# Performance work log

Hardware: AMD Instinct MI355X
Metric: run time of the kernel (lower is better)

The kernel has to match this reference:

```python
import jax, jax.numpy as jnp
import numpy as np


def _bicubic_warp(img, dx, dy):
    """Faithful JAX port of Warp_Object.forward with flag='bicubic'.
    img: [B,C,H,W] float32; dx, dy: [B,1,H,W] pixel displacements.
    Replicates the original tile-order quirk: X/Y are repeated C times along
    dim0 (order c*B+b) while the image is flattened in b*C+c order.
    """
    B, C, H, W = img.shape
    Wm1 = jnp.float32(max(W - 1, 1))
    Hm1 = jnp.float32(max(H - 1, 1))
    xs = jnp.arange(W, dtype=jnp.float32)
    ys = jnp.arange(H, dtype=jnp.float32)
    Xg, Yg = jnp.meshgrid(xs, ys)          # [H,W]
    # normalized grid in [-1,1] as in forward()
    newX = 2.0 * (Xg[None] + dx[:, 0]) / Wm1 - 1.0   # [B,H,W]
    newY = 2.0 * (Yg[None] + dy[:, 0]) / Hm1 - 1.0
    # repeat over channels exactly like X.repeat([C,1,1,1]) (tile order)
    x_map = (jnp.tile(newX, (C, 1, 1)) + 1.0) * Wm1 / 2.0   # [B*C,H,W]
    y_map = (jnp.tile(newY, (C, 1, 1)) + 1.0) * Hm1 / 2.0

    x0 = jnp.floor(x_map)
    y0 = jnp.floor(y_map)
    tx = x_map - x0
    ty = y_map - y0

    def cubic_coeffs(t):
        cm1 = (-t ** 3 + 2.0 * t ** 2 - t) / 2.0
        c0 = (3.0 * t ** 3 - 5.0 * t ** 2 + 2.0) / 2.0
        c1 = (-3.0 * t ** 3 + 4.0 * t ** 2 + t) / 2.0
        c2 = 1.0 - (cm1 + c0 + c1)
        return (cm1, c0, c1, c2)

    cx = cubic_coeffs(tx)
    cy = cubic_coeffs(ty)

    x0i = x0.astype(jnp.int32)
    y0i = y0.astype(jnp.int32)
    xi = [jnp.clip(x0i + o, 0, W - 1) for o in (-1, 0, 1, 2)]
    yi = [jnp.clip(y0i + o, 0, H - 1) for o in (-1, 0, 1, 2)]

    flat = img.reshape(B * C, H, W)
    row = jnp.arange(B * C)[:, None, None]   # per-image base offset

    out = jnp.zeros_like(x_map)
    for j in range(4):            # 4 rows of the 4x4 bicubic stencil
        row_acc = jnp.zeros_like(x_map)
        for i in range(4):
            row_acc = row_acc + cx[i] * flat[row, yi[j], xi[i]]
        out = out + cy[j] * row_acc
    return out.reshape(B, C, H, W)


def setup_inputs() -> dict:
    key = jax.random.key(0)
    k1, k2, k3 = jax.random.split(key, 3)
    B, C, H, W = 4, 3, 512, 512
    input_image = jax.random.normal(k1, (B, C, H, W), dtype=jnp.float32)
    delta_x = jax.random.normal(k2, (B, 1, H, W), dtype=jnp.float32) * 1.5
    delta_y = jax.random.normal(k3, (B, 1, H, W), dtype=jnp.float32) * 1.5
    return {"input_image": input_image, "delta_x": delta_x, "delta_y": delta_y}


def reference(input_image, delta_x, delta_y):
    return _bicubic_warp(input_image, delta_x, delta_y)
```

## Files before the change

kernel.cpp:

```cpp
#include <hip/hip_runtime.h>


constexpr int B = 4, C = 3, H = 512, W = 512;
constexpr int HW = H * W;
constexpr int TH2 = 32, TW = 32;
constexpr int HALO = 6;
constexpr int RS = TH2 + 2 * HALO;
constexpr int LSTC = 48;
constexpr int CHR = LSTC / 4;
constexpr int NCH = RS * CHR;
constexpr int CPW = NCH / 16;
constexpr int TDW = RS * LSTC;
constexpr int NT = 1024;
constexpr int NB = B * (H / TH2) * (W / TW);

typedef float f4 __attribute__((ext_vector_type(4)));
typedef f4 f4u __attribute__((aligned(4)));

typedef const __attribute__((address_space(1))) void* gas_t;
typedef __attribute__((address_space(3))) void* las_t;

__device__ __forceinline__ void gload_lds16(const float* g, float* l) {
    __builtin_amdgcn_global_load_lds((gas_t)g, (las_t)l, 16, 0, 0);
}

__global__ __launch_bounds__(NT, 8)
void warp_bicubic_gen(const float* __restrict__ img,
                      const float* __restrict__ dxp,
                      const float* __restrict__ dyp,
                      float* __restrict__ out)
{
    __shared__ float tile[C][TDW];

    int b   = blockIdx.x;
    int swz = (b & 7) * (NB / 8) + (b >> 3);
    int bd  = swz >> 8;
    int ty  = (swz >> 4) & 15;
    int tx  = swz & 15;
    int yb  = ty * TH2;
    int xb  = tx * TW;
    int cb  = min(max(xb - HALO, 0), W - LSTC);

    int tid  = threadIdx.x;
    int wv   = tid >> 6;
    int lane = tid & 63;
    int ry   = wv * 2 + (lane >> 5);
    int cidx = lane & 31;
    int y    = yb + ry;
    int x    = xb + cidx;
    int pixoff = y * W + x;

    float dxv = __builtin_nontemporal_load(dxp + bd * HW + pixoff);
    float dyv = __builtin_nontemporal_load(dyp + bd * HW + pixoff);

    if (lane < CPW) {
        int chunk = wv * CPW + lane;
        int r  = chunk / CHR;
        int c4 = (chunk - r * CHR) * 4;
        int sr = min(max(yb - HALO + r, 0), H - 1);
        int soff = sr * W + cb + c4;
        const float* g0 = img + (size_t)bd * HW + soff;
        float* l0 = &tile[0][chunk * 4];
        gload_lds16(g0,           l0);
        gload_lds16(g0 + 4 * HW,  l0 + TDW);
        gload_lds16(g0 + 8 * HW,  l0 + 2 * TDW);
    }

    float xm = (float)x + dxv;
    float ym = (float)y + dyv;
    float x0f = floorf(xm), y0f = floorf(ym);
    float ftx = xm - x0f, fty = ym - y0f;
    int x0 = (int)x0f, y0 = (int)y0f;
    int s  = min(max(x0 - 1, 0), W - 4);

    float tx2 = ftx * ftx, tx3 = tx2 * ftx;
    float cx0 = (-tx3 + 2.0f * tx2 - ftx) * 0.5f;
    float cx1 = (3.0f * tx3 - 5.0f * tx2 + 2.0f) * 0.5f;
    float cx2 = (-3.0f * tx3 + 4.0f * tx2 + ftx) * 0.5f;
    float cx3 = 1.0f - (cx0 + cx1 + cx2);

    float ty2 = fty * fty, ty3 = ty2 * fty;
    float cy0 = (-ty3 + 2.0f * ty2 - fty) * 0.5f;
    float cy1 = (3.0f * ty3 - 5.0f * ty2 + 2.0f) * 0.5f;
    float cy2 = (-3.0f * ty3 + 4.0f * ty2 + fty) * 0.5f;
    float cy3 = 1.0f - (cy0 + cy1 + cy2);

    float w0, w1, w2, w3;
    if (__builtin_expect(x0 >= 1 && x0 <= W - 3, 1)) {
        w0 = cx0; w1 = cx1; w2 = cx2; w3 = cx3;
    } else {
        w0 = w1 = w2 = w3 = 0.f;
        const float cxa[4] = {cx0, cx1, cx2, cx3};
#pragma unroll
        for (int o = 0; o < 4; ++o) {
            int xi = min(max(x0 - 1 + o, 0), W - 1);
            int e  = xi - s;
            float cc = cxa[o];
            w0 += (e == 0) ? cc : 0.f;
            w1 += (e == 1) ? cc : 0.f;
            w2 += (e == 2) ? cc : 0.f;
            w3 += (e == 3) ? cc : 0.f;
        }
    }

    unsigned rel = (unsigned)(y0 - (yb - HALO + 1));
    unsigned lsv = (unsigned)(s - cb);
    bool intile = (rel <= (unsigned)(RS - 4)) & (lsv <= (unsigned)(LSTC - 4));
    int lbase = (int)rel * LSTC + (int)lsv;

    __syncthreads();

#pragma unroll
    for (int c = 0; c < C; ++c) {
        int kp = bd + 4 * c;
        const float* __restrict__ tp = &tile[c][0];
        float acc;
        if (__builtin_expect(intile, 1)) {
            const float* rp = tp + lbase;
            float r0 = cy0 * (w0 * rp[0] + w1 * rp[1] + w2 * rp[2] + w3 * rp[3]);
            rp += LSTC;
            float r1 = cy1 * (w0 * rp[0] + w1 * rp[1] + w2 * rp[2] + w3 * rp[3]);
            rp += LSTC;
            float r2 = cy2 * (w0 * rp[0] + w1 * rp[1] + w2 * rp[2] + w3 * rp[3]);
            rp += LSTC;
            float r3 = cy3 * (w0 * rp[0] + w1 * rp[1] + w2 * rp[2] + w3 * rp[3]);
            acc = (r0 + r1) + (r2 + r3);
        } else {
            const float* __restrict__ plane = img + (size_t)kp * HW;
            const float cya[4] = {cy0, cy1, cy2, cy3};
            acc = 0.f;
#pragma unroll
            for (int j = 0; j < 4; ++j) {
                int yi = min(max(y0 - 1 + j, 0), H - 1);
                f4 v = *(const f4u*)(plane + yi * W + s);
                acc += cya[j] * (w0 * v.x + w1 * v.y + w2 * v.z + w3 * v.w);
            }
        }
        __builtin_nontemporal_store(acc, out + (size_t)kp * HW + pixoff);
    }
}

extern "C" void kernel_launch(void* const* d_in, const int* in_sizes, int n_in,
                              void* d_out, int out_size, void* d_ws, size_t ws_size,
                              hipStream_t stream) {
    const float* img = (const float*)d_in[0];
    const float* dx  = (const float*)d_in[1];
    const float* dy  = (const float*)d_in[2];
    float* out = (float*)d_out;

    dim3 block(NT);
    dim3 grid(NB);
    hipLaunchKernelGGL(warp_bicubic_gen, grid, block, 0, stream,
                       img, dx, dy, out);
}
```

Measured before the change: 16.11 us.

## Process two vertically stacked tiles per block with double-buffered LDS staging

Each workgroup now covers two adjacent 32x32 tiles, halving the grid to 512 blocks. Both tiles' image halos are issued to LDS asynchronously up front, into separate buffers. Partial vmcnt waits let the first tile's stencil run while the second tile's loads are still in flight. This aims to hide global-load latency and amortise per-block setup, at the cost of fewer blocks to spread across CUs, reloading the halo rows the two tiles share, and fragile hand-counted waitcnt logic.

```diff
diff --git a/kernel.cpp b/kernel.cpp
--- a/kernel.cpp
+++ b/kernel.cpp
@@ -3,16 +3,16 @@
 
 constexpr int B = 4, C = 3, H = 512, W = 512;
 constexpr int HW = H * W;
-constexpr int TH2 = 32, TW = 32;
+constexpr int TS = 32;
 constexpr int HALO = 6;
-constexpr int RS = TH2 + 2 * HALO;
+constexpr int RS = TS + 2 * HALO;
 constexpr int LSTC = 48;
 constexpr int CHR = LSTC / 4;
 constexpr int NCH = RS * CHR;
 constexpr int CPW = NCH / 16;
 constexpr int TDW = RS * LSTC;
 constexpr int NT = 1024;
-constexpr int NB = B * (H / TH2) * (W / TW);
+constexpr int NB = 512;
 
 typedef float f4 __attribute__((ext_vector_type(4)));
 typedef f4 f4u __attribute__((aligned(4)));
@@ -24,48 +24,17 @@
     __builtin_amdgcn_global_load_lds((gas_t)g, (las_t)l, 16, 0, 0);
 }
 
-__global__ __launch_bounds__(NT, 8)
-void warp_bicubic_gen(const float* __restrict__ img,
-                      const float* __restrict__ dxp,
-                      const float* __restrict__ dyp,
-                      float* __restrict__ out)
-{
-    __shared__ float tile[C][TDW];
-
-    int b   = blockIdx.x;
-    int swz = (b & 7) * (NB / 8) + (b >> 3);
-    int bd  = swz >> 8;
-    int ty  = (swz >> 4) & 15;
-    int tx  = swz & 15;
-    int yb  = ty * TH2;
-    int xb  = tx * TW;
-    int cb  = min(max(xb - HALO, 0), W - LSTC);
-
-    int tid  = threadIdx.x;
-    int wv   = tid >> 6;
-    int lane = tid & 63;
-    int ry   = wv * 2 + (lane >> 5);
-    int cidx = lane & 31;
-    int y    = yb + ry;
-    int x    = xb + cidx;
-    int pixoff = y * W + x;
-
-    float dxv = __builtin_nontemporal_load(dxp + bd * HW + pixoff);
-    float dyv = __builtin_nontemporal_load(dyp + bd * HW + pixoff);
-
-    if (lane < CPW) {
-        int chunk = wv * CPW + lane;
-        int r  = chunk / CHR;
-        int c4 = (chunk - r * CHR) * 4;
-        int sr = min(max(yb - HALO + r, 0), H - 1);
-        int soff = sr * W + cb + c4;
-        const float* g0 = img + (size_t)bd * HW + soff;
-        float* l0 = &tile[0][chunk * 4];
-        gload_lds16(g0,           l0);
-        gload_lds16(g0 + 4 * HW,  l0 + TDW);
-        gload_lds16(g0 + 8 * HW,  l0 + 2 * TDW);
-    }
-
+struct Coef {
+    float w0, w1, w2, w3;
+    float cy0, cy1, cy2, cy3;
+    int   lbase;
+    bool  intile;
+    int   y0, s;
+};
+
+__device__ __forceinline__ Coef make_coef(int x, int y, float dxv, float dyv,
+                                          int yb, int cb) {
+    Coef cf;
     float xm = (float)x + dxv;
     float ym = (float)y + dyv;
     float x0f = floorf(xm), y0f = floorf(ym);
@@ -76,20 +45,19 @@
     float tx2 = ftx * ftx, tx3 = tx2 * ftx;
     float cx0 = (-tx3 + 2.0f * tx2 - ftx) * 0.5f;
     float cx1 = (3.0f * tx3 - 5.0f * tx2 + 2.0f) * 0.5f;
-    float cx2 = (-3.0f * tx3 + 4.0f * tx2 + ftx) * 0.5f;
+    float cx2 = (-tx3 * 3.0f + 4.0f * tx2 + ftx) * 0.5f;
     float cx3 = 1.0f - (cx0 + cx1 + cx2);
 
     float ty2 = fty * fty, ty3 = ty2 * fty;
-    float cy0 = (-ty3 + 2.0f * ty2 - fty) * 0.5f;
-    float cy1 = (3.0f * ty3 - 5.0f * ty2 + 2.0f) * 0.5f;
-    float cy2 = (-3.0f * ty3 + 4.0f * ty2 + fty) * 0.5f;
-    float cy3 = 1.0f - (cy0 + cy1 + cy2);
-
-    float w0, w1, w2, w3;
+    cf.cy0 = (-ty3 + 2.0f * ty2 - fty) * 0.5f;
+    cf.cy1 = (3.0f * ty3 - 5.0f * ty2 + 2.0f) * 0.5f;
+    cf.cy2 = (-3.0f * ty3 + 4.0f * ty2 + fty) * 0.5f;
+    cf.cy3 = 1.0f - (cf.cy0 + cf.cy1 + cf.cy2);
+
     if (__builtin_expect(x0 >= 1 && x0 <= W - 3, 1)) {
-        w0 = cx0; w1 = cx1; w2 = cx2; w3 = cx3;
+        cf.w0 = cx0; cf.w1 = cx1; cf.w2 = cx2; cf.w3 = cx3;
     } else {
-        w0 = w1 = w2 = w3 = 0.f;
+        float w0 = 0.f, w1 = 0.f, w2 = 0.f, w3 = 0.f;
         const float cxa[4] = {cx0, cx1, cx2, cx3};
 #pragma unroll
         for (int o = 0; o < 4; ++o) {
@@ -101,42 +69,122 @@
             w2 += (e == 2) ? cc : 0.f;
             w3 += (e == 3) ? cc : 0.f;
         }
+        cf.w0 = w0; cf.w1 = w1; cf.w2 = w2; cf.w3 = w3;
     }
 
     unsigned rel = (unsigned)(y0 - (yb - HALO + 1));
     unsigned lsv = (unsigned)(s - cb);
-    bool intile = (rel <= (unsigned)(RS - 4)) & (lsv <= (unsigned)(LSTC - 4));
-    int lbase = (int)rel * LSTC + (int)lsv;
-
-    __syncthreads();
+    cf.intile = (rel <= (unsigned)(RS - 4)) & (lsv <= (unsigned)(LSTC - 4));
+    cf.lbase  = (int)rel * LSTC + (int)lsv;
+    cf.y0 = y0; cf.s = s;
+    return cf;
+}
+
+__device__ __forceinline__ float stencil1(const float* __restrict__ tp,
+                                          const Coef& cf,
+                                          const float* __restrict__ plane) {
+    if (__builtin_expect(cf.intile, 1)) {
+        const float* rp = tp + cf.lbase;
+        float r0 = cf.cy0 * (cf.w0 * rp[0] + cf.w1 * rp[1] + cf.w2 * rp[2] + cf.w3 * rp[3]);
+        rp += LSTC;
+        float r1 = cf.cy1 * (cf.w0 * rp[0] + cf.w1 * rp[1] + cf.w2 * rp[2] + cf.w3 * rp[3]);
+        rp += LSTC;
+        float r2 = cf.cy2 * (cf.w0 * rp[0] + cf.w1 * rp[1] + cf.w2 * rp[2] + cf.w3 * rp[3]);
+        rp += LSTC;
+        float r3 = cf.cy3 * (cf.w0 * rp[0] + cf.w1 * rp[1] + cf.w2 * rp[2] + cf.w3 * rp[3]);
+        return (r0 + r1) + (r2 + r3);
+    } else {
+        const float cya[4] = {cf.cy0, cf.cy1, cf.cy2, cf.cy3};
+        float acc = 0.f;
+#pragma unroll
+        for (int j = 0; j < 4; ++j) {
+            int yi = min(max(cf.y0 - 1 + j, 0), H - 1);
+            f4 v = *(const f4u*)(plane + yi * W + cf.s);
+            acc += cya[j] * (cf.w0 * v.x + cf.w1 * v.y + cf.w2 * v.z + cf.w3 * v.w);
+        }
+        return acc;
+    }
+}
+
+__device__ __forceinline__ void stage_tile(const float* __restrict__ img, int bd,
+                                           int yb, int cb, float* dst,
+                                           int wv, int lane) {
+    if (lane < CPW) {
+        int chunk = wv * CPW + lane;
+        int r  = chunk / CHR;
+        int c4 = (chunk - r * CHR) * 4;
+        int sr = min(max(yb - HALO + r, 0), H - 1);
+        int soff = sr * W + cb + c4;
+        const float* g0 = img + (size_t)bd * HW + soff;
+        float* l0 = dst + chunk * 4;
+        gload_lds16(g0,          l0);
+        gload_lds16(g0 + 4 * HW, l0 + TDW);
+        gload_lds16(g0 + 8 * HW, l0 + 2 * TDW);
+    }
+}
+
+__global__ __launch_bounds__(NT, 8)
+void warp_bicubic_2t(const float* __restrict__ img,
+                     const float* __restrict__ dxp,
+                     const float* __restrict__ dyp,
+                     float* __restrict__ out)
+{
+    __shared__ float tile[2][C * TDW];
+
+    int b   = blockIdx.x;
+    int swz = (b & 7) * (NB / 8) + (b >> 3);
+    int bd  = swz >> 7;
+    int rem = swz & 127;
+    int typ = rem >> 4;
+    int txx = rem & 15;
+    int xb  = txx * TS;
+    int cb  = min(max(xb - HALO, 0), W - LSTC);
+    int yb0 = typ * 2 * TS;
+    int yb1 = yb0 + TS;
+
+    int tid  = threadIdx.x;
+    int wv   = tid >> 6;
+    int lane = tid & 63;
+    int ry   = wv * 2 + (lane >> 5);
+    int cidx = lane & 31;
+    int x    = xb + cidx;
+    int po0  = (yb0 + ry) * W + x;
+    int po1  = (yb1 + ry) * W + x;
+
+    float dx0 = __builtin_nontemporal_load(dxp + bd * HW + po0);
+    float dy0 = __builtin_nontemporal_load(dyp + bd * HW + po0);
+    float dx1 = __builtin_nontemporal_load(dxp + bd * HW + po1);
+    float dy1 = __builtin_nontemporal_load(dyp + bd * HW + po1);
+
+    Coef c0 = make_coef(x, yb0 + ry, dx0, dy0, yb0, cb);
+    Coef c1 = make_coef(x, yb1 + ry, dx1, dy1, yb1, cb);
+    __builtin_amdgcn_sched_barrier(0);
+
+    stage_tile(img, bd, yb0, cb, &tile[0][0], wv, lane);
+    __builtin_amdgcn_sched_barrier(0);
+    stage_tile(img, bd, yb1, cb, &tile[1][0], wv, lane);
+    __builtin_amdgcn_sched_barrier(0);
+
+    asm volatile("s_waitcnt vmcnt(3)" ::: "memory");
+    __builtin_amdgcn_sched_barrier(0);
+    __builtin_amdgcn_s_barrier();
 
 #pragma unroll
     for (int c = 0; c < C; ++c) {
         int kp = bd + 4 * c;
-        const float* __restrict__ tp = &tile[c][0];
-        float acc;
-        if (__builtin_expect(intile, 1)) {
-            const float* rp = tp + lbase;
-            float r0 = cy0 * (w0 * rp[0] + w1 * rp[1] + w2 * rp[2] + w3 * rp[3]);
-            rp += LSTC;
-            float r1 = cy1 * (w0 * rp[0] + w1 * rp[1] + w2 * rp[2] + w3 * rp[3]);
-            rp += LSTC;
-            float r2 = cy2 * (w0 * rp[0] + w1 * rp[1] + w2 * rp[2] + w3 * rp[3]);
-            rp += LSTC;
-            float r3 = cy3 * (w0 * rp[0] + w1 * rp[1] + w2 * rp[2] + w3 * rp[3]);
-            acc = (r0 + r1) + (r2 + r3);
-        } else {
-            const float* __restrict__ plane = img + (size_t)kp * HW;
-            const float cya[4] = {cy0, cy1, cy2, cy3};
-            acc = 0.f;
-#pragma unroll
-            for (int j = 0; j < 4; ++j) {
-                int yi = min(max(y0 - 1 + j, 0), H - 1);
-                f4 v = *(const f4u*)(plane + yi * W + s);
-                acc += cya[j] * (w0 * v.x + w1 * v.y + w2 * v.z + w3 * v.w);
-            }
-        }
-        __builtin_nontemporal_store(acc, out + (size_t)kp * HW + pixoff);
+        float acc = stencil1(&tile[0][c * TDW], c0, img + (size_t)kp * HW);
+        __builtin_nontemporal_store(acc, out + (size_t)kp * HW + po0);
+    }
+
+    asm volatile("s_waitcnt vmcnt(3)" ::: "memory");
+    __builtin_amdgcn_sched_barrier(0);
+    __builtin_amdgcn_s_barrier();
+
+#pragma unroll
+    for (int c = 0; c < C; ++c) {
+        int kp = bd + 4 * c;
+        float acc = stencil1(&tile[1][c * TDW], c1, img + (size_t)kp * HW);
+        __builtin_nontemporal_store(acc, out + (size_t)kp * HW + po1);
     }
 }
 
@@ -150,6 +198,6 @@
 
     dim3 block(NT);
     dim3 grid(NB);
-    hipLaunchKernelGGL(warp_bicubic_gen, grid, block, 0, stream,
+    hipLaunchKernelGGL(warp_bicubic_2t, grid, block, 0, stream,
                        img, dx, dy, out);
 }
```

After: 16.74 us. 1.04x slower.

## Use taller 64x32 tiles with two output pixels per thread

Applied to the files above, without the earlier changes.

Doubles the tile height from 32 to 64 rows so each 1024-thread block covers 64x32 pixels, with every thread computing two output rows spaced two apart. The shared halo is now amortised over twice as many output rows, which cuts redundant LDS staging of image rows and halves the block count. The cost is more registers per thread and fewer, larger blocks, which can reduce occupancy and leave the GPU less evenly loaded.

```diff
diff --git a/kernel.cpp b/kernel.cpp
--- a/kernel.cpp
+++ b/kernel.cpp
@@ -3,16 +3,17 @@
 
 constexpr int B = 4, C = 3, H = 512, W = 512;
 constexpr int HW = H * W;
-constexpr int TH2 = 32, TW = 32;
+constexpr int TSY = 64, TSX = 32;
 constexpr int HALO = 6;
-constexpr int RS = TH2 + 2 * HALO;
+constexpr int RS = TSY + 2 * HALO;
 constexpr int LSTC = 48;
 constexpr int CHR = LSTC / 4;
 constexpr int NCH = RS * CHR;
 constexpr int CPW = NCH / 16;
 constexpr int TDW = RS * LSTC;
+constexpr int NPOS = 2;
 constexpr int NT = 1024;
-constexpr int NB = B * (H / TH2) * (W / TW);
+constexpr int NB = B * (H / TSY) * (W / TSX);
 
 typedef float f4 __attribute__((ext_vector_type(4)));
 typedef f4 f4u __attribute__((aligned(4)));
@@ -25,33 +26,36 @@
 }
 
 __global__ __launch_bounds__(NT, 8)
-void warp_bicubic_gen(const float* __restrict__ img,
-                      const float* __restrict__ dxp,
-                      const float* __restrict__ dyp,
-                      float* __restrict__ out)
+void warp_bicubic_tall(const float* __restrict__ img,
+                       const float* __restrict__ dxp,
+                       const float* __restrict__ dyp,
+                       float* __restrict__ out)
 {
     __shared__ float tile[C][TDW];
 
     int b   = blockIdx.x;
     int swz = (b & 7) * (NB / 8) + (b >> 3);
-    int bd  = swz >> 8;
-    int ty  = (swz >> 4) & 15;
-    int tx  = swz & 15;
-    int yb  = ty * TH2;
-    int xb  = tx * TW;
+    int bd  = swz >> 7;
+    int rem = swz & 127;
+    int ysr = rem >> 4;
+    int xsc = rem & 15;
+    int yb  = ysr * TSY;
+    int xb  = xsc * TSX;
     int cb  = min(max(xb - HALO, 0), W - LSTC);
 
     int tid  = threadIdx.x;
     int wv   = tid >> 6;
     int lane = tid & 63;
-    int ry   = wv * 2 + (lane >> 5);
-    int cidx = lane & 31;
-    int y    = yb + ry;
-    int x    = xb + cidx;
-    int pixoff = y * W + x;
+    int ryb  = wv * 4 + (lane >> 5);
+    int x    = xb + (lane & 31);
 
-    float dxv = __builtin_nontemporal_load(dxp + bd * HW + pixoff);
-    float dyv = __builtin_nontemporal_load(dyp + bd * HW + pixoff);
+    float dxa[NPOS], dya[NPOS];
+#pragma unroll
+    for (int p = 0; p < NPOS; ++p) {
+        int po = (yb + ryb + 2 * p) * W + x;
+        dxa[p] = __builtin_nontemporal_load(dxp + bd * HW + po);
+        dya[p] = __builtin_nontemporal_load(dyp + bd * HW + po);
+    }
 
     if (lane < CPW) {
         int chunk = wv * CPW + lane;
@@ -61,52 +65,60 @@
         int soff = sr * W + cb + c4;
         const float* g0 = img + (size_t)bd * HW + soff;
         float* l0 = &tile[0][chunk * 4];
-        gload_lds16(g0,           l0);
-        gload_lds16(g0 + 4 * HW,  l0 + TDW);
-        gload_lds16(g0 + 8 * HW,  l0 + 2 * TDW);
+        gload_lds16(g0,          l0);
+        gload_lds16(g0 + 4 * HW, l0 + TDW);
+        gload_lds16(g0 + 8 * HW, l0 + 2 * TDW);
     }
 
-    float xm = (float)x + dxv;
-    float ym = (float)y + dyv;
-    float x0f = floorf(xm), y0f = floorf(ym);
-    float ftx = xm - x0f, fty = ym - y0f;
-    int x0 = (int)x0f, y0 = (int)y0f;
-    int s  = min(max(x0 - 1, 0), W - 4);
+    float wx[NPOS][4], cyw[NPOS][4];
+    int   lbase[NPOS];
+    unsigned relv[NPOS], lsv[NPOS];
+    bool  intile[NPOS];
+#pragma unroll
+    for (int p = 0; p < NPOS; ++p) {
+        int y = yb + ryb + 2 * p;
+        float xm = (float)x + dxa[p];
+        float ym = (float)y + dya[p];
+        float x0f = floorf(xm), y0f = floorf(ym);
+        float ftx = xm - x0f, fty = ym - y0f;
+        int x0 = (int)x0f, y0 = (int)y0f;
+        int s  = min(max(x0 - 1, 0), W - 4);
 
-    float tx2 = ftx * ftx, tx3 = tx2 * ftx;
-    float cx0 = (-tx3 + 2.0f * tx2 - ftx) * 0.5f;
-    float cx1 = (3.0f * tx3 - 5.0f * tx2 + 2.0f) * 0.5f;
-    float cx2 = (-3.0f * tx3 + 4.0f * tx2 + ftx) * 0.5f;
-    float cx3 = 1.0f - (cx0 + cx1 + cx2);
+        float tx2 = ftx * ftx, tx3 = tx2 * ftx;
+        float cx0 = (-tx3 + 2.0f * tx2 - ftx) * 0.5f;
+        float cx1 = (3.0f * tx3 - 5.0f * tx2 + 2.0f) * 0.5f;
+        float cx2 = (-3.0f * tx3 + 4.0f * tx2 + ftx) * 0.5f;
+        float cx3 = 1.0f - (cx0 + cx1 + cx2);
 
-    float ty2 = fty * fty, ty3 = ty2 * fty;
-    float cy0 = (-ty3 + 2.0f * ty2 - fty) * 0.5f;
-    float cy1 = (3.0f * ty3 - 5.0f * ty2 + 2.0f) * 0.5f;
-    float cy2 = (-3.0f * ty3 + 4.0f * ty2 + fty) * 0.5f;
-    float cy3 = 1.0f - (cy0 + cy1 + cy2);
+        float ty2 = fty * fty, ty3 = ty2 * fty;
+        cyw[p][0] = (-ty3 + 2.0f * ty2 - fty) * 0.5f;
+        cyw[p][1] = (3.0f * ty3 - 5.0f * ty2 + 2.0f) * 0.5f;
+        cyw[p][2] = (-3.0f * ty3 + 4.0f * ty2 + fty) * 0.5f;
+        cyw[p][3] = 1.0f - (cyw[p][0] + cyw[p][1] + cyw[p][2]);
 
-    float w0, w1, w2, w3;
-    if (__builtin_expect(x0 >= 1 && x0 <= W - 3, 1)) {
-        w0 = cx0; w1 = cx1; w2 = cx2; w3 = cx3;
-    } else {
-        w0 = w1 = w2 = w3 = 0.f;
-        const float cxa[4] = {cx0, cx1, cx2, cx3};
+        if (__builtin_expect(x0 >= 1 && x0 <= W - 3, 1)) {
+            wx[p][0] = cx0; wx[p][1] = cx1; wx[p][2] = cx2; wx[p][3] = cx3;
+        } else {
+            float w0 = 0.f, w1 = 0.f, w2 = 0.f, w3 = 0.f;
+            const float cxa[4] = {cx0, cx1, cx2, cx3};
 #pragma unroll
-        for (int o = 0; o < 4; ++o) {
-            int xi = min(max(x0 - 1 + o, 0), W - 1);
-            int e  = xi - s;
-            float cc = cxa[o];
-            w0 += (e == 0) ? cc : 0.f;
-            w1 += (e == 1) ? cc : 0.f;
-            w2 += (e == 2) ? cc : 0.f;
-            w3 += (e == 3) ? cc : 0.f;
+            for (int o = 0; o < 4; ++o) {
+                int xi = min(max(x0 - 1 + o, 0), W - 1);
+                int e  = xi - s;
+                float cc = cxa[o];
+                w0 += (e == 0) ? cc : 0.f;
+                w1 += (e == 1) ? cc : 0.f;
+                w2 += (e == 2) ? cc : 0.f;
+                w3 += (e == 3) ? cc : 0.f;
+            }
+            wx[p][0] = w0; wx[p][1] = w1; wx[p][2] = w2; wx[p][3] = w3;
         }
+
+        relv[p]  = (unsigned)(y0 - (yb - HALO + 1));
+        lsv[p]   = (unsigned)(s - cb);
+        intile[p] = (relv[p] <= (unsigned)(RS - 4)) & (lsv[p] <= (unsigned)(LSTC - 4));
+        lbase[p] = (int)relv[p] * LSTC + (int)lsv[p];
     }
-
-    unsigned rel = (unsigned)(y0 - (yb - HALO + 1));
-    unsigned lsv = (unsigned)(s - cb);
-    bool intile = (rel <= (unsigned)(RS - 4)) & (lsv <= (unsigned)(LSTC - 4));
-    int lbase = (int)rel * LSTC + (int)lsv;
 
     __syncthreads();
 
@@ -114,29 +126,34 @@
     for (int c = 0; c < C; ++c) {
         int kp = bd + 4 * c;
         const float* __restrict__ tp = &tile[c][0];
-        float acc;
-        if (__builtin_expect(intile, 1)) {
-            const float* rp = tp + lbase;
-            float r0 = cy0 * (w0 * rp[0] + w1 * rp[1] + w2 * rp[2] + w3 * rp[3]);
-            rp += LSTC;
-            float r1 = cy1 * (w0 * rp[0] + w1 * rp[1] + w2 * rp[2] + w3 * rp[3]);
-            rp += LSTC;
-            float r2 = cy2 * (w0 * rp[0] + w1 * rp[1] + w2 * rp[2] + w3 * rp[3]);
-            rp += LSTC;
-            float r3 = cy3 * (w0 * rp[0] + w1 * rp[1] + w2 * rp[2] + w3 * rp[3]);
-            acc = (r0 + r1) + (r2 + r3);
-        } else {
-            const float* __restrict__ plane = img + (size_t)kp * HW;
-            const float cya[4] = {cy0, cy1, cy2, cy3};
-            acc = 0.f;
 #pragma unroll
-            for (int j = 0; j < 4; ++j) {
-                int yi = min(max(y0 - 1 + j, 0), H - 1);
-                f4 v = *(const f4u*)(plane + yi * W + s);
-                acc += cya[j] * (w0 * v.x + w1 * v.y + w2 * v.z + w3 * v.w);
+        for (int p = 0; p < NPOS; ++p) {
+            int po = (yb + ryb + 2 * p) * W + x;
+            float acc;
+            if (__builtin_expect(intile[p], 1)) {
+                const float* rp = tp + lbase[p];
+                float r0 = cyw[p][0] * (wx[p][0]*rp[0] + wx[p][1]*rp[1] + wx[p][2]*rp[2] + wx[p][3]*rp[3]);
+                rp += LSTC;
+                float r1 = cyw[p][1] * (wx[p][0]*rp[0] + wx[p][1]*rp[1] + wx[p][2]*rp[2] + wx[p][3]*rp[3]);
+                rp += LSTC;
+                float r2 = cyw[p][2] * (wx[p][0]*rp[0] + wx[p][1]*rp[1] + wx[p][2]*rp[2] + wx[p][3]*rp[3]);
+                rp += LSTC;
+                float r3 = cyw[p][3] * (wx[p][0]*rp[0] + wx[p][1]*rp[1] + wx[p][2]*rp[2] + wx[p][3]*rp[3]);
+                acc = (r0 + r1) + (r2 + r3);
+            } else {
+                const float* __restrict__ plane = img + (size_t)kp * HW;
+                int y0 = (int)relv[p] + (yb - HALO + 1);
+                int s  = (int)lsv[p] + cb;
+                acc = 0.f;
+#pragma unroll
+                for (int j = 0; j < 4; ++j) {
+                    int yi = min(max(y0 - 1 + j, 0), H - 1);
+                    f4 v = *(const f4u*)(plane + yi * W + s);
+                    acc += cyw[p][j] * (wx[p][0]*v.x + wx[p][1]*v.y + wx[p][2]*v.z + wx[p][3]*v.w);
+                }
             }
+            __builtin_nontemporal_store(acc, out + (size_t)kp * HW + po);
         }
-        __builtin_nontemporal_store(acc, out + (size_t)kp * HW + pixoff);
     }
 }
 
@@ -150,6 +167,6 @@
 
     dim3 block(NT);
     dim3 grid(NB);
-    hipLaunchKernelGGL(warp_bicubic_gen, grid, block, 0, stream,
+    hipLaunchKernelGGL(warp_bicubic_tall, grid, block, 0, stream,
                        img, dx, dy, out);
 }
```

After: 16.55 us. +2.7%, slower.
